# Kernel tuning notes

Measured on AMD Instinct MI355X. Metric: run time of the kernel, lower is better.

## Reference

```python
import jax, jax.numpy as jnp
import numpy as np

B, N, D, H = 2, 2048, 1024, 16
DH = D // H


def setup_inputs() -> dict:
    key = jax.random.key(0)
    ks = jax.random.split(key, 5)
    s = 0.02
    return {
        "x": jax.random.normal(ks[0], (B, N, D), dtype=jnp.float32),
        "Wq": jax.random.normal(ks[1], (D, D), dtype=jnp.float32) * s,
        "Wk": jax.random.normal(ks[2], (D, D), dtype=jnp.float32) * s,
        "Wv": jax.random.normal(ks[3], (D, D), dtype=jnp.float32) * s,
        "Wo": jax.random.normal(ks[4], (D, D), dtype=jnp.float32) * s,
        "bo": jnp.zeros((D,), dtype=jnp.float32),
    }


def reference(x, Wq, Wk, Wv, Wo, bo):
    b, n, d = x.shape
    # linear projections (torch Linear: y = x @ W.T), split into heads -> [b,h,n,dh]
    def proj(W):
        return jnp.einsum('bnd,ed->bne', x, W).reshape(b, n, H, DH).transpose(0, 2, 1, 3)
    q, k, v = proj(Wq), proj(Wk), proj(Wv)
    scores = jnp.einsum('bhqd,bhkd->bhqk', q, k)  # [b,h,n,n]
    causal = jnp.triu(jnp.ones((n, n), dtype=bool), k=1)
    scores = jnp.where(causal, -jnp.inf, scores)
    # NOTE: module scales by 1/sqrt(num_key_tokens), not 1/sqrt(d_head)
    w = jax.nn.softmax(scores / jnp.sqrt(jnp.float32(n)), axis=-1)
    ctx = jnp.einsum('bhqk,bhkd->bhqd', w, v)
    ctx = ctx.transpose(0, 2, 1, 3).reshape(b, n, d)
    return jnp.einsum('bnd,ed->bne', ctx, Wo) + bo
```

## Files before the change

kernel.cpp:

```cpp
#include <hip/hip_runtime.h>
#include <hip/hip_bf16.h>

typedef __attribute__((ext_vector_type(8))) short bf16x8;
typedef __attribute__((ext_vector_type(4))) float f32x4;
typedef unsigned short u16;

__device__ __forceinline__ u16 f2bf(float f) {
  union { float f; unsigned int u; } v; v.f = f;
  return (u16)((v.u + 0x7fffu + ((v.u >> 16) & 1u)) >> 16);
}
__device__ __forceinline__ unsigned int pack_bf2(float f0, float f1) {
  union { float f; unsigned int u; } a, b; a.f = f0; b.f = f1;
  return __builtin_amdgcn_perm(b.u + 0x8000u, a.u + 0x8000u, 0x07060302u);
}

#define GLOAD_LDS16(g, l) __builtin_amdgcn_global_load_lds( \
    (const __attribute__((address_space(1))) void*)(g),     \
    (__attribute__((address_space(3))) void*)(l), 16, 0, 0)

__global__ __launch_bounds__(256) void conv_all(const float* __restrict__ x,
                                                const float* __restrict__ wq, const float* __restrict__ wk,
                                                const float* __restrict__ wv, const float* __restrict__ wo,
                                                u16* __restrict__ xb, u16* __restrict__ qo, u16* __restrict__ ko,
                                                u16* __restrict__ vo, u16* __restrict__ oo) {
  int y = blockIdx.y;
  const float* src; u16* dst;
  if (y < 4) { src = x + (size_t)y * 1048576; dst = xb + (size_t)y * 1048576; }
  else if (y == 4) { src = wq; dst = qo; }
  else if (y == 5) { src = wk; dst = ko; }
  else if (y == 6) { src = wv; dst = vo; }
  else { src = wo; dst = oo; }
  int i = (blockIdx.x * 256 + threadIdx.x) * 4;
  float4 v = *(const float4*)(src + i);
  ushort4 o;
  o.x = f2bf(v.x); o.y = f2bf(v.y); o.z = f2bf(v.z); o.w = f2bf(v.w);
  *(ushort4*)(dst + i) = o;
}

__device__ __forceinline__ void gemm_main(const u16* __restrict__ A, const u16* __restrict__ W,
                                          u16* As, u16* Bs, int m0, int n0, int K,
                                          f32x4 acc[4][4]) {
  int tid = threadIdx.x, wave = tid >> 6, lane = tid & 63;
  int lane15 = lane & 15, quad = lane >> 4;
  int wm = (wave >> 1) * 64, wn = (wave & 1) * 64;
  for (int k0 = 0; k0 < K; k0 += 64) {
    __syncthreads();
#pragma unroll
    for (int i = 0; i < 4; i++) {
      int rbase = wave * 32 + i * 8;
      int rloc = rbase + (lane >> 3);
      int ca = ((lane & 7) ^ (rloc & 7)) * 8;
      GLOAD_LDS16(A + (size_t)(m0 + rloc) * K + k0 + ca, As + rbase * 64);
      GLOAD_LDS16(W + (size_t)(n0 + rloc) * K + k0 + ca, Bs + rbase * 64);
    }
    __syncthreads();
#pragma unroll
    for (int kc = 0; kc < 2; kc++) {
      bf16x8 a[4], b[4];
#pragma unroll
      for (int mi = 0; mi < 4; mi++) {
        int m = wm + mi * 16 + lane15;
        a[mi] = *(const bf16x8*)(As + m * 64 + (((kc * 4 + quad) ^ (m & 7)) * 8));
      }
#pragma unroll
      for (int ni = 0; ni < 4; ni++) {
        int n = wn + ni * 16 + lane15;
        b[ni] = *(const bf16x8*)(Bs + n * 64 + (((kc * 4 + quad) ^ (n & 7)) * 8));
      }
#pragma unroll
      for (int mi = 0; mi < 4; mi++)
#pragma unroll
        for (int ni = 0; ni < 4; ni++)
          acc[mi][ni] = __builtin_amdgcn_mfma_f32_16x16x32_bf16(a[mi], b[ni], acc[mi][ni], 0, 0, 0);
    }
  }
}

__global__ __launch_bounds__(256, 3) void gemm_qkv(const u16* __restrict__ xb,
                                                   const u16* __restrict__ wq, const u16* __restrict__ wk,
                                                   const u16* __restrict__ wv,
                                                   u16* __restrict__ Qb, u16* __restrict__ Kb,
                                                   u16* __restrict__ Vtg) {
  __shared__ __align__(16) u16 As[128 * 64];
  __shared__ __align__(16) u16 Bs[128 * 64];
  const int K = 1024;
  int z = blockIdx.z;
  const u16* W = (z == 0) ? wq : (z == 1) ? wk : wv;
  int m0 = blockIdx.x * 128, n0 = blockIdx.y * 128;
  f32x4 acc[4][4];
#pragma unroll
  for (int i = 0; i < 4; i++)
#pragma unroll
    for (int j = 0; j < 4; j++) acc[i][j] = (f32x4){0.f, 0.f, 0.f, 0.f};
  gemm_main(xb, W, As, Bs, m0, n0, K, acc);

  int tid = threadIdx.x, wave = tid >> 6, lane = tid & 63;
  int lane15 = lane & 15, quad = lane >> 4;
  int wm = (wave >> 1) * 64, wn = (wave & 1) * 64;
  const float kQs = 0.022097086912079608f * 1.4426950408889634f;
  if (z < 2) {
    u16* Out = z ? Kb : Qb;
    float sc = z ? 1.0f : kQs;
#pragma unroll
    for (int mi = 0; mi < 4; mi++)
#pragma unroll
      for (int ni = 0; ni < 4; ni++) {
        int row = m0 + wm + mi * 16 + quad * 4;
        int col = n0 + wn + ni * 16 + lane15;
#pragma unroll
        for (int r = 0; r < 4; r++)
          Out[(size_t)(row + r) * 1024 + col] = f2bf(acc[mi][ni][r] * sc);
      }
  } else {
#pragma unroll
    for (int mi = 0; mi < 4; mi++)
#pragma unroll
      for (int ni = 0; ni < 4; ni++) {
        int row = m0 + wm + mi * 16 + quad * 4;
        int col = n0 + wn + ni * 16 + lane15;
        int bb = row >> 11, nn = row & 2047;
        ushort4 o;
        o.x = f2bf(acc[mi][ni][0]); o.y = f2bf(acc[mi][ni][1]);
        o.z = f2bf(acc[mi][ni][2]); o.w = f2bf(acc[mi][ni][3]);
        *(ushort4*)&Vtg[(size_t)(bb * 1024 + col) * 2048 + nn] = o;
      }
  }
}

__global__ __launch_bounds__(256, 2) void gemm_out(const u16* __restrict__ A, const u16* __restrict__ W,
                                                   float* __restrict__ Of, const float* __restrict__ bias) {
  __shared__ __align__(16) u16 As[128 * 64];
  __shared__ __align__(16) u16 Bs[64 * 64];
  const int K = 1024;
  int m0 = blockIdx.x * 128, n0 = blockIdx.y * 64;
  int tid = threadIdx.x, wave = tid >> 6, lane = tid & 63;
  int lane15 = lane & 15, quad = lane >> 4;
  int wm = (wave >> 1) * 64, wn = (wave & 1) * 32;
  f32x4 acc[4][2];
#pragma unroll
  for (int i = 0; i < 4; i++)
#pragma unroll
    for (int j = 0; j < 2; j++) acc[i][j] = (f32x4){0.f, 0.f, 0.f, 0.f};
  for (int k0 = 0; k0 < K; k0 += 64) {
    __syncthreads();
#pragma unroll
    for (int i = 0; i < 4; i++) {
      int rbase = wave * 32 + i * 8;
      int rloc = rbase + (lane >> 3);
      int ca = ((lane & 7) ^ (rloc & 7)) * 8;
      GLOAD_LDS16(A + (size_t)(m0 + rloc) * K + k0 + ca, As + rbase * 64);
    }
#pragma unroll
    for (int i = 0; i < 2; i++) {
      int rbase = wave * 16 + i * 8;
      int rloc = rbase + (lane >> 3);
      int ca = ((lane & 7) ^ (rloc & 7)) * 8;
      GLOAD_LDS16(W + (size_t)(n0 + rloc) * K + k0 + ca, Bs + rbase * 64);
    }
    __syncthreads();
#pragma unroll
    for (int kc = 0; kc < 2; kc++) {
      bf16x8 a[4], b[2];
#pragma unroll
      for (int mi = 0; mi < 4; mi++) {
        int m = wm + mi * 16 + lane15;
        a[mi] = *(const bf16x8*)(As + m * 64 + (((kc * 4 + quad) ^ (m & 7)) * 8));
      }
#pragma unroll
      for (int ni = 0; ni < 2; ni++) {
        int n = wn + ni * 16 + lane15;
        b[ni] = *(const bf16x8*)(Bs + n * 64 + (((kc * 4 + quad) ^ (n & 7)) * 8));
      }
#pragma unroll
      for (int mi = 0; mi < 4; mi++)
#pragma unroll
        for (int ni = 0; ni < 2; ni++)
          acc[mi][ni] = __builtin_amdgcn_mfma_f32_16x16x32_bf16(a[mi], b[ni], acc[mi][ni], 0, 0, 0);
    }
  }
#pragma unroll
  for (int mi = 0; mi < 4; mi++)
#pragma unroll
    for (int ni = 0; ni < 2; ni++) {
      int row = m0 + wm + mi * 16 + quad * 4;
      int col = n0 + wn + ni * 16 + lane15;
#pragma unroll
      for (int r = 0; r < 4; r++)
        Of[(size_t)(row + r) * 1024 + col] = acc[mi][ni][r] + bias[col];
    }
}

__global__ __launch_bounds__(256, 2) void attn3(const u16* __restrict__ Q, const u16* __restrict__ Kg,
                                                const u16* __restrict__ Vtg, u16* __restrict__ ctx) {
  __shared__ __align__(16) u16 KsL[128 * 64];
  __shared__ __align__(16) u16 VtsL[64 * 128];
  __shared__ __align__(16) u16 Ps2[128 * 128];
  int tid = threadIdx.x, wave = tid >> 6, lane = tid & 63;
  int lane15 = lane & 15, quad = lane >> 4;

  int bid = blockIdx.x;
  int pairIdx = bid & 255, half = bid >> 8;
  int p8 = pairIdx & 7, bh = pairIdx >> 3;
  int qt = half ? (15 - p8) : p8;
  int b = bh >> 4, h = bh & 15;
  int qbase = qt * 128;

  bf16x8 qb[2][2];
#pragma unroll
  for (int mi = 0; mi < 2; mi++)
#pragma unroll
    for (int kc = 0; kc < 2; kc++)
      qb[mi][kc] = *(const bf16x8*)&Q[(size_t)(b * 2048 + qbase + wave * 32 + mi * 16 + lane15) * 1024 +
                                      h * 64 + kc * 32 + quad * 8];

  f32x4 oacc[4][2];
#pragma unroll
  for (int c4 = 0; c4 < 4; c4++)
#pragma unroll
    for (int mi = 0; mi < 2; mi++) oacc[c4][mi] = (f32x4){0.f, 0.f, 0.f, 0.f};
  float mrow[2] = {-3.0e38f, -3.0e38f}, lrow[2] = {0.f, 0.f};

  for (int t = 0; t <= qt; ++t) {
    int k0 = t * 128;
    __syncthreads();
#pragma unroll
    for (int i = 0; i < 4; i++) {
      int rbase = wave * 32 + i * 8;
      int rk = rbase + (lane >> 3);
      int ca = ((lane & 7) ^ (rk & 7)) * 8;
      GLOAD_LDS16(&Kg[(size_t)(b * 2048 + k0 + rk) * 1024 + h * 64 + ca], KsL + rbase * 64);
      int vbase = wave * 16 + i * 4;
      int rv = vbase + (lane >> 4);
      int cv = ((lane & 15) ^ (rv & 15)) * 8;
      GLOAD_LDS16(&Vtg[(size_t)(b * 1024 + h * 64 + rv) * 2048 + k0 + cv], VtsL + vbase * 128);
    }
    __syncthreads();

    f32x4 s[2][8];
#pragma unroll
    for (int ct = 0; ct < 8; ct++) {
      int kr = ct * 16 + lane15;
      bf16x8 ka0 = *(const bf16x8*)(KsL + kr * 64 + ((quad ^ (kr & 7)) * 8));
      bf16x8 ka1 = *(const bf16x8*)(KsL + kr * 64 + (((4 + quad) ^ (kr & 7)) * 8));
#pragma unroll
      for (int mi = 0; mi < 2; mi++) {
        f32x4 z = (f32x4){0.f, 0.f, 0.f, 0.f};
        z = __builtin_amdgcn_mfma_f32_16x16x32_bf16(ka0, qb[mi][0], z, 0, 0, 0);
        z = __builtin_amdgcn_mfma_f32_16x16x32_bf16(ka1, qb[mi][1], z, 0, 0, 0);
        s[mi][ct] = z;
      }
    }

    bool diag = (t == qt);
#pragma unroll
    for (int mi = 0; mi < 2; mi++) {
      if (diag) {
        int ql = wave * 32 + mi * 16 + lane15;
#pragma unroll
        for (int ct = 0; ct < 8; ct++)
#pragma unroll
          for (int r = 0; r < 4; r++)
            if (ct * 16 + quad * 4 + r > ql) s[mi][ct][r] = -3.0e38f;
      }
      float mx = mrow[mi];
#pragma unroll
      for (int ct = 0; ct < 8; ct++)
#pragma unroll
        for (int r = 0; r < 4; r++) mx = fmaxf(mx, s[mi][ct][r]);
      mx = fmaxf(mx, __shfl_xor(mx, 16));
      mx = fmaxf(mx, __shfl_xor(mx, 32));
      float sum = 0.f;
#pragma unroll
      for (int ct = 0; ct < 8; ct++)
#pragma unroll
        for (int r = 0; r < 4; r++) {
          float p = __builtin_amdgcn_exp2f(s[mi][ct][r] - mx);
          s[mi][ct][r] = p; sum += p;
        }
      sum += __shfl_xor(sum, 16);
      sum += __shfl_xor(sum, 32);
      float alpha = __builtin_amdgcn_exp2f(mrow[mi] - mx);
      lrow[mi] = lrow[mi] * alpha + sum;
      mrow[mi] = mx;
#pragma unroll
      for (int c4 = 0; c4 < 4; c4++)
#pragma unroll
        for (int r = 0; r < 4; r++) oacc[c4][mi][r] *= alpha;
      int prow = wave * 32 + mi * 16 + lane15;
      int sw = (lane15 & 7) << 1;
#pragma unroll
      for (int ct = 0; ct < 8; ct++) {
        unsigned int lo = pack_bf2(s[mi][ct][0], s[mi][ct][1]);
        unsigned int hi = pack_bf2(s[mi][ct][2], s[mi][ct][3]);
        int c8 = (ct * 4 + quad) ^ sw;
        *(uint2*)&Ps2[prow * 128 + c8 * 4] = (uint2){lo, hi};
      }
    }

#pragma unroll
    for (int kc = 0; kc < 4; kc++) {
      bf16x8 pb[2];
#pragma unroll
      for (int mi = 0; mi < 2; mi++) {
        int prow = wave * 32 + mi * 16 + lane15;
        int c8 = (kc * 8 + quad * 2) ^ ((lane15 & 7) << 1);
        pb[mi] = *(const bf16x8*)&Ps2[prow * 128 + c8 * 4];
      }
      int cb = kc * 4 + quad;
#pragma unroll
      for (int c4 = 0; c4 < 4; c4++) {
        int dh = c4 * 16 + lane15;
        bf16x8 va = *(const bf16x8*)(VtsL + dh * 128 + ((cb ^ (dh & 15)) * 8));
        oacc[c4][0] = __builtin_amdgcn_mfma_f32_16x16x32_bf16(va, pb[0], oacc[c4][0], 0, 0, 0);
        oacc[c4][1] = __builtin_amdgcn_mfma_f32_16x16x32_bf16(va, pb[1], oacc[c4][1], 0, 0, 0);
      }
    }
  }

#pragma unroll
  for (int mi = 0; mi < 2; mi++) {
    float inv = 1.0f / lrow[mi];
    size_t rowoff = (size_t)(b * 2048 + qbase + wave * 32 + mi * 16 + lane15) * 1024 + h * 64;
#pragma unroll
    for (int c4 = 0; c4 < 4; c4++) {
      ushort4 o;
      o.x = f2bf(oacc[c4][mi][0] * inv); o.y = f2bf(oacc[c4][mi][1] * inv);
      o.z = f2bf(oacc[c4][mi][2] * inv); o.w = f2bf(oacc[c4][mi][3] * inv);
      *(ushort4*)&ctx[rowoff + c4 * 16 + quad * 4] = o;
    }
  }
}

extern "C" void kernel_launch(void* const* d_in, const int* in_sizes, int n_in,
                              void* d_out, int out_size, void* d_ws, size_t ws_size,
                              hipStream_t stream) {
  const float* x  = (const float*)d_in[0];
  const float* Wq = (const float*)d_in[1];
  const float* Wk = (const float*)d_in[2];
  const float* Wv = (const float*)d_in[3];
  const float* Wo = (const float*)d_in[4];
  const float* bo = (const float*)d_in[5];
  float* out = (float*)d_out;
  char* ws = (char*)d_ws;
  const size_t MB = 1024 * 1024;
  u16* xb   = (u16*)(ws);
  u16* wqb  = (u16*)(ws +  8 * MB);
  u16* wkb  = (u16*)(ws + 10 * MB);
  u16* wvb  = (u16*)(ws + 12 * MB);
  u16* wob  = (u16*)(ws + 14 * MB);
  u16* Qb   = (u16*)(ws + 16 * MB);
  u16* Kb   = (u16*)(ws + 24 * MB);
  u16* Vtg  = (u16*)(ws + 32 * MB);
  u16* ctxb = (u16*)(ws + 40 * MB);

  conv_all<<<dim3(1024, 8), 256, 0, stream>>>(x, Wq, Wk, Wv, Wo, xb, wqb, wkb, wvb, wob);
  gemm_qkv<<<dim3(32, 8, 3), 256, 0, stream>>>(xb, wqb, wkb, wvb, Qb, Kb, Vtg);
  attn3<<<dim3(512), 256, 0, stream>>>(Qb, Kb, Vtg, ctxb);
  gemm_out<<<dim3(32, 16), 256, 0, stream>>>(ctxb, wob, out, bo);
}
```

Baseline: 179.4 us.

## Restructure causal attention with paired query strips and double-buffered K/V tiles

Rewrites the attention kernel so each block handles two 64-row query strips (tile g and tile 31-g), which balances causal work evenly across blocks. K and V tiles are double-buffered so the next tile loads while the current one is computed, with one barrier per iteration. It also swaps MFMA operand order in the Q/K and output GEMMs so each lane stores contiguous ushort4 or float4 vectors instead of scalar writes. The costs are smaller 64-wide key tiles, more loop iterations, and a bias load per output vector.

```diff
diff --git a/kernel.cpp b/kernel.cpp
--- a/kernel.cpp
+++ b/kernel.cpp
@@ -37,6 +37,7 @@
   *(ushort4*)(dst + i) = o;
 }
 
+template <bool SW>
 __device__ __forceinline__ void gemm_main(const u16* __restrict__ A, const u16* __restrict__ W,
                                           u16* As, u16* Bs, int m0, int n0, int K,
                                           f32x4 acc[4][4]) {
@@ -71,7 +72,8 @@
       for (int mi = 0; mi < 4; mi++)
 #pragma unroll
         for (int ni = 0; ni < 4; ni++)
-          acc[mi][ni] = __builtin_amdgcn_mfma_f32_16x16x32_bf16(a[mi], b[ni], acc[mi][ni], 0, 0, 0);
+          acc[mi][ni] = SW ? __builtin_amdgcn_mfma_f32_16x16x32_bf16(b[ni], a[mi], acc[mi][ni], 0, 0, 0)
+                           : __builtin_amdgcn_mfma_f32_16x16x32_bf16(a[mi], b[ni], acc[mi][ni], 0, 0, 0);
     }
   }
 }
@@ -92,26 +94,29 @@
   for (int i = 0; i < 4; i++)
 #pragma unroll
     for (int j = 0; j < 4; j++) acc[i][j] = (f32x4){0.f, 0.f, 0.f, 0.f};
-  gemm_main(xb, W, As, Bs, m0, n0, K, acc);
 
   int tid = threadIdx.x, wave = tid >> 6, lane = tid & 63;
   int lane15 = lane & 15, quad = lane >> 4;
   int wm = (wave >> 1) * 64, wn = (wave & 1) * 64;
   const float kQs = 0.022097086912079608f * 1.4426950408889634f;
+
   if (z < 2) {
+    gemm_main<true>(xb, W, As, Bs, m0, n0, K, acc);
     u16* Out = z ? Kb : Qb;
     float sc = z ? 1.0f : kQs;
 #pragma unroll
     for (int mi = 0; mi < 4; mi++)
 #pragma unroll
       for (int ni = 0; ni < 4; ni++) {
-        int row = m0 + wm + mi * 16 + quad * 4;
-        int col = n0 + wn + ni * 16 + lane15;
-#pragma unroll
-        for (int r = 0; r < 4; r++)
-          Out[(size_t)(row + r) * 1024 + col] = f2bf(acc[mi][ni][r] * sc);
+        int token = m0 + wm + mi * 16 + lane15;
+        int fb = n0 + wn + ni * 16 + quad * 4;
+        ushort4 o;
+        o.x = f2bf(acc[mi][ni][0] * sc); o.y = f2bf(acc[mi][ni][1] * sc);
+        o.z = f2bf(acc[mi][ni][2] * sc); o.w = f2bf(acc[mi][ni][3] * sc);
+        *(ushort4*)&Out[(size_t)token * 1024 + fb] = o;
       }
   } else {
+    gemm_main<false>(xb, W, As, Bs, m0, n0, K, acc);
 #pragma unroll
     for (int mi = 0; mi < 4; mi++)
 #pragma unroll
@@ -175,158 +180,152 @@
       for (int mi = 0; mi < 4; mi++)
 #pragma unroll
         for (int ni = 0; ni < 2; ni++)
-          acc[mi][ni] = __builtin_amdgcn_mfma_f32_16x16x32_bf16(a[mi], b[ni], acc[mi][ni], 0, 0, 0);
+          acc[mi][ni] = __builtin_amdgcn_mfma_f32_16x16x32_bf16(b[ni], a[mi], acc[mi][ni], 0, 0, 0);
     }
   }
 #pragma unroll
   for (int mi = 0; mi < 4; mi++)
 #pragma unroll
     for (int ni = 0; ni < 2; ni++) {
-      int row = m0 + wm + mi * 16 + quad * 4;
-      int col = n0 + wn + ni * 16 + lane15;
-#pragma unroll
-      for (int r = 0; r < 4; r++)
-        Of[(size_t)(row + r) * 1024 + col] = acc[mi][ni][r] + bias[col];
-    }
-}
-
-__global__ __launch_bounds__(256, 2) void attn3(const u16* __restrict__ Q, const u16* __restrict__ Kg,
+      int token = m0 + wm + mi * 16 + lane15;
+      int fb = n0 + wn + ni * 16 + quad * 4;
+      float4 bb = *(const float4*)&bias[fb];
+      float4 o;
+      o.x = acc[mi][ni][0] + bb.x; o.y = acc[mi][ni][1] + bb.y;
+      o.z = acc[mi][ni][2] + bb.z; o.w = acc[mi][ni][3] + bb.w;
+      *(float4*)&Of[(size_t)token * 1024 + fb] = o;
+    }
+}
+
+__global__ __launch_bounds__(256, 2) void attn4(const u16* __restrict__ Q, const u16* __restrict__ Kg,
                                                 const u16* __restrict__ Vtg, u16* __restrict__ ctx) {
-  __shared__ __align__(16) u16 KsL[128 * 64];
-  __shared__ __align__(16) u16 VtsL[64 * 128];
-  __shared__ __align__(16) u16 Ps2[128 * 128];
+  __shared__ __align__(16) u16 Ks[2][64 * 64];
+  __shared__ __align__(16) u16 Vts[2][64 * 64];
+  __shared__ __align__(16) u16 Ps[128 * 64];
   int tid = threadIdx.x, wave = tid >> 6, lane = tid & 63;
   int lane15 = lane & 15, quad = lane >> 4;
 
-  int bid = blockIdx.x;
-  int pairIdx = bid & 255, half = bid >> 8;
-  int p8 = pairIdx & 7, bh = pairIdx >> 3;
-  int qt = half ? (15 - p8) : p8;
+  int g = blockIdx.x, bh = blockIdx.y;
   int b = bh >> 4, h = bh & 15;
-  int qbase = qt * 128;
+  int tA = g, tB = 31 - g;
+  int baseA = g * 64, baseB = (31 - g) * 64;
 
   bf16x8 qb[2][2];
 #pragma unroll
-  for (int mi = 0; mi < 2; mi++)
-#pragma unroll
-    for (int kc = 0; kc < 2; kc++)
-      qb[mi][kc] = *(const bf16x8*)&Q[(size_t)(b * 2048 + qbase + wave * 32 + mi * 16 + lane15) * 1024 +
-                                      h * 64 + kc * 32 + quad * 8];
-
-  f32x4 oacc[4][2];
-#pragma unroll
-  for (int c4 = 0; c4 < 4; c4++)
-#pragma unroll
-    for (int mi = 0; mi < 2; mi++) oacc[c4][mi] = (f32x4){0.f, 0.f, 0.f, 0.f};
+  for (int kc = 0; kc < 2; kc++) {
+    qb[0][kc] = *(const bf16x8*)&Q[(size_t)(b * 2048 + baseA + wave * 16 + lane15) * 1024 +
+                                   h * 64 + kc * 32 + quad * 8];
+    qb[1][kc] = *(const bf16x8*)&Q[(size_t)(b * 2048 + baseB + wave * 16 + lane15) * 1024 +
+                                   h * 64 + kc * 32 + quad * 8];
+  }
+
+  f32x4 oacc[2][4];
+#pragma unroll
+  for (int st = 0; st < 2; st++)
+#pragma unroll
+    for (int c4 = 0; c4 < 4; c4++) oacc[st][c4] = (f32x4){0.f, 0.f, 0.f, 0.f};
   float mrow[2] = {-3.0e38f, -3.0e38f}, lrow[2] = {0.f, 0.f};
 
-  for (int t = 0; t <= qt; ++t) {
-    int k0 = t * 128;
-    __syncthreads();
-#pragma unroll
-    for (int i = 0; i < 4; i++) {
-      int rbase = wave * 32 + i * 8;
+  auto stage = [&](int t, int d) {
+    int tb = t * 64;
+#pragma unroll
+    for (int i = 0; i < 2; i++) {
+      int rbase = wave * 16 + i * 8;
       int rk = rbase + (lane >> 3);
       int ca = ((lane & 7) ^ (rk & 7)) * 8;
-      GLOAD_LDS16(&Kg[(size_t)(b * 2048 + k0 + rk) * 1024 + h * 64 + ca], KsL + rbase * 64);
-      int vbase = wave * 16 + i * 4;
-      int rv = vbase + (lane >> 4);
-      int cv = ((lane & 15) ^ (rv & 15)) * 8;
-      GLOAD_LDS16(&Vtg[(size_t)(b * 1024 + h * 64 + rv) * 2048 + k0 + cv], VtsL + vbase * 128);
-    }
-    __syncthreads();
-
-    f32x4 s[2][8];
-#pragma unroll
-    for (int ct = 0; ct < 8; ct++) {
+      GLOAD_LDS16(&Kg[(size_t)(b * 2048 + tb + rk) * 1024 + h * 64 + ca], &Ks[d][rbase * 64]);
+      GLOAD_LDS16(&Vtg[(size_t)(b * 1024 + h * 64 + rk) * 2048 + tb + ca], &Vts[d][rbase * 64]);
+    }
+  };
+
+  int sw = (lane15 & 7) << 1;
+
+  auto compute_strip = [&](int st, bool diag, int d) {
+    f32x4 s[4];
+#pragma unroll
+    for (int ct = 0; ct < 4; ct++) {
       int kr = ct * 16 + lane15;
-      bf16x8 ka0 = *(const bf16x8*)(KsL + kr * 64 + ((quad ^ (kr & 7)) * 8));
-      bf16x8 ka1 = *(const bf16x8*)(KsL + kr * 64 + (((4 + quad) ^ (kr & 7)) * 8));
-#pragma unroll
-      for (int mi = 0; mi < 2; mi++) {
-        f32x4 z = (f32x4){0.f, 0.f, 0.f, 0.f};
-        z = __builtin_amdgcn_mfma_f32_16x16x32_bf16(ka0, qb[mi][0], z, 0, 0, 0);
-        z = __builtin_amdgcn_mfma_f32_16x16x32_bf16(ka1, qb[mi][1], z, 0, 0, 0);
-        s[mi][ct] = z;
-      }
-    }
-
-    bool diag = (t == qt);
-#pragma unroll
-    for (int mi = 0; mi < 2; mi++) {
-      if (diag) {
-        int ql = wave * 32 + mi * 16 + lane15;
-#pragma unroll
-        for (int ct = 0; ct < 8; ct++)
-#pragma unroll
-          for (int r = 0; r < 4; r++)
-            if (ct * 16 + quad * 4 + r > ql) s[mi][ct][r] = -3.0e38f;
-      }
-      float mx = mrow[mi];
-#pragma unroll
-      for (int ct = 0; ct < 8; ct++)
-#pragma unroll
-        for (int r = 0; r < 4; r++) mx = fmaxf(mx, s[mi][ct][r]);
-      mx = fmaxf(mx, __shfl_xor(mx, 16));
-      mx = fmaxf(mx, __shfl_xor(mx, 32));
-      float sum = 0.f;
-#pragma unroll
-      for (int ct = 0; ct < 8; ct++)
-#pragma unroll
-        for (int r = 0; r < 4; r++) {
-          float p = __builtin_amdgcn_exp2f(s[mi][ct][r] - mx);
-          s[mi][ct][r] = p; sum += p;
-        }
-      sum += __shfl_xor(sum, 16);
-      sum += __shfl_xor(sum, 32);
-      float alpha = __builtin_amdgcn_exp2f(mrow[mi] - mx);
-      lrow[mi] = lrow[mi] * alpha + sum;
-      mrow[mi] = mx;
-#pragma unroll
-      for (int c4 = 0; c4 < 4; c4++)
-#pragma unroll
-        for (int r = 0; r < 4; r++) oacc[c4][mi][r] *= alpha;
-      int prow = wave * 32 + mi * 16 + lane15;
-      int sw = (lane15 & 7) << 1;
-#pragma unroll
-      for (int ct = 0; ct < 8; ct++) {
-        unsigned int lo = pack_bf2(s[mi][ct][0], s[mi][ct][1]);
-        unsigned int hi = pack_bf2(s[mi][ct][2], s[mi][ct][3]);
-        int c8 = (ct * 4 + quad) ^ sw;
-        *(uint2*)&Ps2[prow * 128 + c8 * 4] = (uint2){lo, hi};
-      }
-    }
-
-#pragma unroll
-    for (int kc = 0; kc < 4; kc++) {
-      bf16x8 pb[2];
-#pragma unroll
-      for (int mi = 0; mi < 2; mi++) {
-        int prow = wave * 32 + mi * 16 + lane15;
-        int c8 = (kc * 8 + quad * 2) ^ ((lane15 & 7) << 1);
-        pb[mi] = *(const bf16x8*)&Ps2[prow * 128 + c8 * 4];
-      }
-      int cb = kc * 4 + quad;
+      const u16* kp = &Ks[d][kr * 64];
+      bf16x8 ka0 = *(const bf16x8*)(kp + ((quad ^ (kr & 7)) * 8));
+      bf16x8 ka1 = *(const bf16x8*)(kp + (((4 + quad) ^ (kr & 7)) * 8));
+      f32x4 z = (f32x4){0.f, 0.f, 0.f, 0.f};
+      z = __builtin_amdgcn_mfma_f32_16x16x32_bf16(ka0, qb[st][0], z, 0, 0, 0);
+      z = __builtin_amdgcn_mfma_f32_16x16x32_bf16(ka1, qb[st][1], z, 0, 0, 0);
+      s[ct] = z;
+    }
+    if (diag) {
+      int ql = wave * 16 + lane15;
+#pragma unroll
+      for (int ct = 0; ct < 4; ct++)
+#pragma unroll
+        for (int r = 0; r < 4; r++)
+          if (ct * 16 + quad * 4 + r > ql) s[ct][r] = -3.0e38f;
+    }
+    float mx = mrow[st];
+#pragma unroll
+    for (int ct = 0; ct < 4; ct++)
+#pragma unroll
+      for (int r = 0; r < 4; r++) mx = fmaxf(mx, s[ct][r]);
+    mx = fmaxf(mx, __shfl_xor(mx, 16));
+    mx = fmaxf(mx, __shfl_xor(mx, 32));
+    float sum = 0.f;
+#pragma unroll
+    for (int ct = 0; ct < 4; ct++)
+#pragma unroll
+      for (int r = 0; r < 4; r++) {
+        float p = __builtin_amdgcn_exp2f(s[ct][r] - mx);
+        s[ct][r] = p; sum += p;
+      }
+    sum += __shfl_xor(sum, 16);
+    sum += __shfl_xor(sum, 32);
+    float alpha = __builtin_amdgcn_exp2f(mrow[st] - mx);
+    lrow[st] = lrow[st] * alpha + sum;
+    mrow[st] = mx;
+#pragma unroll
+    for (int c4 = 0; c4 < 4; c4++)
+#pragma unroll
+      for (int r = 0; r < 4; r++) oacc[st][c4][r] *= alpha;
+    int prow = st * 64 + wave * 16 + lane15;
+#pragma unroll
+    for (int ct = 0; ct < 4; ct++) {
+      unsigned int lo = pack_bf2(s[ct][0], s[ct][1]);
+      unsigned int hi = pack_bf2(s[ct][2], s[ct][3]);
+      int u = (ct * 4 + quad) ^ sw;
+      *(uint2*)&Ps[prow * 64 + u * 4] = (uint2){lo, hi};
+    }
+#pragma unroll
+    for (int kc = 0; kc < 2; kc++) {
+      int up = (kc * 8 + quad * 2) ^ sw;
+      bf16x8 pb = *(const bf16x8*)&Ps[prow * 64 + up * 4];
 #pragma unroll
       for (int c4 = 0; c4 < 4; c4++) {
         int dh = c4 * 16 + lane15;
-        bf16x8 va = *(const bf16x8*)(VtsL + dh * 128 + ((cb ^ (dh & 15)) * 8));
-        oacc[c4][0] = __builtin_amdgcn_mfma_f32_16x16x32_bf16(va, pb[0], oacc[c4][0], 0, 0, 0);
-        oacc[c4][1] = __builtin_amdgcn_mfma_f32_16x16x32_bf16(va, pb[1], oacc[c4][1], 0, 0, 0);
-      }
-    }
-  }
-
-#pragma unroll
-  for (int mi = 0; mi < 2; mi++) {
-    float inv = 1.0f / lrow[mi];
-    size_t rowoff = (size_t)(b * 2048 + qbase + wave * 32 + mi * 16 + lane15) * 1024 + h * 64;
+        bf16x8 va = *(const bf16x8*)&Vts[d][dh * 64 + (((kc * 4 + quad) ^ (dh & 7)) * 8)];
+        oacc[st][c4] = __builtin_amdgcn_mfma_f32_16x16x32_bf16(va, pb, oacc[st][c4], 0, 0, 0);
+      }
+    }
+  };
+
+  stage(0, 0);
+  for (int t = 0; t <= tB; ++t) {
+    __syncthreads();
+    if (t < tB) stage(t + 1, (t + 1) & 1);
+    int d = t & 1;
+    if (t <= tA) compute_strip(0, t == tA, d);
+    compute_strip(1, t == tB, d);
+  }
+
+#pragma unroll
+  for (int st = 0; st < 2; st++) {
+    float inv = 1.0f / lrow[st];
+    int qs = (st ? baseB : baseA) + wave * 16 + lane15;
+    size_t off = (size_t)(b * 2048 + qs) * 1024 + h * 64;
 #pragma unroll
     for (int c4 = 0; c4 < 4; c4++) {
       ushort4 o;
-      o.x = f2bf(oacc[c4][mi][0] * inv); o.y = f2bf(oacc[c4][mi][1] * inv);
-      o.z = f2bf(oacc[c4][mi][2] * inv); o.w = f2bf(oacc[c4][mi][3] * inv);
-      *(ushort4*)&ctx[rowoff + c4 * 16 + quad * 4] = o;
+      o.x = f2bf(oacc[st][c4][0] * inv); o.y = f2bf(oacc[st][c4][1] * inv);
+      o.z = f2bf(oacc[st][c4][2] * inv); o.w = f2bf(oacc[st][c4][3] * inv);
+      *(ushort4*)&ctx[off + c4 * 16 + quad * 4] = o;
     }
   }
 }
@@ -355,6 +354,6 @@
 
   conv_all<<<dim3(1024, 8), 256, 0, stream>>>(x, Wq, Wk, Wv, Wo, xb, wqb, wkb, wvb, wob);
   gemm_qkv<<<dim3(32, 8, 3), 256, 0, stream>>>(xb, wqb, wkb, wvb, Qb, Kb, Vtg);
-  attn3<<<dim3(512), 256, 0, stream>>>(Qb, Kb, Vtg, ctxb);
+  attn4<<<dim3(16, 32), 256, 0, stream>>>(Qb, Kb, Vtg, ctxb);
   gemm_out<<<dim3(32, 16), 256, 0, stream>>>(ctxb, wob, out, bo);
 }
```

Result: no change. 180.8 us (+0.8%).
